# Performance work log

Measured on AMD Instinct MI355X. Metric: run time of the kernel, lower is better.

Reference implementation:

```python
import jax, jax.numpy as jnp
import numpy as np

B, S, D = 4, 2048, 2048


def setup_inputs() -> dict:
    key = jax.random.key(0)
    ks = jax.random.split(key, 9)
    scale = 1.0 / np.sqrt(D)
    x = jax.random.normal(ks[0], (B, S, D), dtype=jnp.float32)
    # causal mask, broadcast to [B, S, S]; 0 -> masked
    mask = jnp.broadcast_to(jnp.tril(jnp.ones((S, S), dtype=jnp.int32)), (B, S, S))
    Wq = jax.random.normal(ks[1], (D, D), dtype=jnp.float32) * scale
    Wk = jax.random.normal(ks[2], (D, D), dtype=jnp.float32) * scale
    Wv = jax.random.normal(ks[3], (D, D), dtype=jnp.float32) * scale
    Wp = jax.random.normal(ks[4], (D, D), dtype=jnp.float32) * scale
    bq = jnp.zeros((D,), jnp.float32)
    bk = jnp.zeros((D,), jnp.float32)
    bv = jnp.zeros((D,), jnp.float32)
    bp = jnp.zeros((D,), jnp.float32)
    return {"x": x, "mask": mask, "Wq": Wq, "bq": bq, "Wk": Wk, "bk": bk,
            "Wv": Wv, "bv": bv, "Wp": Wp, "bp": bp}


def reference(x, mask, Wq, bq, Wk, bk, Wv, bv, Wp, bp):
    # single-head scaled dot-product attention (cache=None path, eval mode)
    d_k = x.shape[-1]
    inv_std = 1.0 / jnp.sqrt(jnp.asarray(d_k, x.dtype))
    q = jnp.einsum('bsd,ed->bse', x, Wq) + bq  # nn.Linear: x @ W^T + b
    k = jnp.einsum('bsd,ed->bse', x, Wk) + bk
    v = jnp.einsum('bsd,ed->bse', x, Wv) + bv
    scores = jnp.einsum('bqd,bkd->bqk', q, k) * inv_std  # [B,S,S]
    scores = jnp.where(mask == 0, jnp.asarray(-jnp.inf, scores.dtype), scores)
    attn = jax.nn.softmax(scores, axis=-1)
    ctx = jnp.einsum('bqk,bkd->bqd', attn, v)
    out = jnp.einsum('bsd,ed->bse', ctx, Wp) + bp
    return out
```

## Files before the change

kernel.cpp:

```cpp
#include <hip/hip_runtime.h>
#include <hip/hip_bf16.h>
#include <type_traits>
#include <math.h>


typedef __bf16 bf16x8_t __attribute__((ext_vector_type(8)));
typedef float f32x4_t __attribute__((ext_vector_type(4)));
typedef unsigned short u16x8_t __attribute__((ext_vector_type(8)));

__device__ inline unsigned short f2bf(float f) {
  unsigned int u = __builtin_bit_cast(unsigned int, f);
  unsigned int r = u + 0x7fffu + ((u >> 16) & 1u);
  return (unsigned short)(r >> 16);
}

__device__ inline void gl2lds16(const unsigned short* g, unsigned short* l) {
  __builtin_amdgcn_global_load_lds(
      (const __attribute__((address_space(1))) unsigned int*)g,
      (__attribute__((address_space(3))) unsigned int*)l, 16, 0, 0);
}

__device__ __forceinline__ bf16x8_t ldf(const unsigned short* p) {
  return __builtin_bit_cast(bf16x8_t, *(const u16x8_t*)p);
}

#define MF(a_, b_, c_) \
  (c_) = __builtin_amdgcn_mfma_f32_16x16x32_bf16((a_), (b_), (c_), 0, 0, 0)
#define SB0() __builtin_amdgcn_sched_barrier(0)
#define BAR()                         \
  do {                                \
    SB0();                            \
    __builtin_amdgcn_s_barrier();     \
    SB0();                            \
  } while (0)
#define LGK0()                                  \
  do {                                          \
    asm volatile("s_waitcnt lgkmcnt(0)");       \
    SB0();                                      \
  } while (0)
#define VM4()                                   \
  do {                                          \
    asm volatile("s_waitcnt vmcnt(4)");         \
    SB0();                                      \
  } while (0)
#define VM6()                                   \
  do {                                          \
    asm volatile("s_waitcnt vmcnt(6)");         \
    SB0();                                      \
  } while (0)
#define PRIO(x) __builtin_amdgcn_s_setprio(x)

__global__ __launch_bounds__(256) void cast_f32_bf16(
    const float* __restrict__ in, unsigned short* __restrict__ out, long n4) {
  long i = blockIdx.x * 256L + threadIdx.x;
  if (i >= n4) return;
  float4 f = ((const float4*)in)[i];
  ushort4 u;
  u.x = f2bf(f.x); u.y = f2bf(f.y); u.z = f2bf(f.z); u.w = f2bf(f.w);
  ((ushort4*)out)[i] = u;
}

__global__ __launch_bounds__(256) void cast_w4(
    const float* __restrict__ w0, const float* __restrict__ w1,
    const float* __restrict__ w2, const float* __restrict__ w3,
    unsigned short* __restrict__ o0, unsigned short* __restrict__ o1,
    unsigned short* __restrict__ o2, unsigned short* __restrict__ o3,
    long n4) {
  long i = blockIdx.x * 256L + threadIdx.x;
  if (i >= n4) return;
  const float* in; unsigned short* out;
  switch (blockIdx.y) {
    case 0: in = w0; out = o0; break;
    case 1: in = w1; out = o1; break;
    case 2: in = w2; out = o2; break;
    default: in = w3; out = o3; break;
  }
  float4 f = ((const float4*)in)[i];
  ushort4 u;
  u.x = f2bf(f.x); u.y = f2bf(f.y); u.z = f2bf(f.z); u.w = f2bf(f.w);
  ((ushort4*)out)[i] = u;
}

__device__ __forceinline__ void g256_kloop(
    const unsigned short* __restrict__ A, const unsigned short* __restrict__ B,
    int K, int Keff, unsigned short* smem, f32x4_t (&acc)[8][4]) {
  const int tid = threadIdx.x;
  const int lane = tid & 63;
  const int wave = tid >> 6;
  const int wr = wave >> 2;
  const int wc = wave & 3;
  const int fr = lane & 15;
  const int q4 = lane >> 4;
  const int s0 = (q4 ^ (fr & 7)) * 8;
  const int s1 = ((q4 + 4) ^ (fr & 7)) * 8;
  const size_t rowK =
      (size_t)(wave * 8 + (lane >> 3)) * (size_t)K +
      (size_t)(((lane & 7) ^ ((lane >> 3) & 7)) * 8);
  const size_t K64 = (size_t)64 * K;
  const size_t K128 = (size_t)128 * K;
  const int wofs = wave * 512;
  const int NT = Keff >> 6;
  const int aoff = wr * 8192 + fr * 64;
  const int boff = 16384 + (wc >> 1) * 8192 + (wc & 1) * 4096 + fr * 64;

#define STG(gp_, lh_)                        \
  do {                                       \
    const unsigned short* g_ = (gp_) + rowK; \
    gl2lds16(g_, (lh_) + wofs);              \
    gl2lds16(g_ + K64, (lh_) + 4096 + wofs); \
  } while (0)

#define MFMA8(mb_, af_)                          \
  _Pragma("unroll")                              \
  for (int n = 0; n < 4; ++n) {                  \
    MF(af_[0][0], bfr[n][0], acc[(mb_)][n]);     \
    MF(af_[0][1], bfr[n][1], acc[(mb_)][n]);     \
    MF(af_[1][0], bfr[n][0], acc[(mb_) + 1][n]); \
    MF(af_[1][1], bfr[n][1], acc[(mb_) + 1][n]); \
  }

#define RDA(dst_, base_, mo_)                          \
  _Pragma("unroll")                                    \
  for (int m = 0; m < 2; ++m) {                        \
    dst_[m][0] = ldf((base_) + (m + (mo_)) * 1024 + s0); \
    dst_[m][1] = ldf((base_) + (m + (mo_)) * 1024 + s1); \
  }

  STG(A, smem);
  STG(A + K128, smem + 8192);
  STG(B, smem + 16384);
  STG(B + K128, smem + 24576);
  STG(B + 64, smem + 32768 + 16384);
  STG(B + K128 + 64, smem + 32768 + 24576);
  STG(A + 64, smem + 32768);
  VM6();
  BAR();

  bf16x8_t bfr[4][2], a01[2][2], a23[2][2], a45[2][2], a67[2][2];
  {
    const unsigned short* Bh = smem + boff;
    const unsigned short* Ah = smem + aoff;
#pragma unroll
    for (int n = 0; n < 4; ++n) {
      bfr[n][0] = ldf(Bh + n * 1024 + s0);
      bfr[n][1] = ldf(Bh + n * 1024 + s1);
    }
    RDA(a01, Ah, 0);
  }

  for (int kt = 0; kt < NT; ++kt) {
    unsigned short* bc = smem + ((kt & 1) << 15);
    unsigned short* nb = smem + (((kt + 1) & 1) << 15);
    const unsigned short* Ahc = bc + aoff;
    const unsigned short* Ahn = nb + aoff;
    const unsigned short* Bhn = nb + boff;
    int k1 = (kt + 1) << 6; if (k1 >= Keff) k1 -= Keff;
    int k2 = (kt + 2) << 6; if (k2 >= Keff) k2 -= Keff;

    RDA(a23, Ahc, 2);
    STG(A + K128 + k1, nb + 8192);
    BAR();
    PRIO(1);
    MFMA8(0, a01);
    PRIO(0);
    BAR();

    RDA(a45, Ahc, 4);
    STG(B + k2, bc + 16384);
    BAR();
    PRIO(1);
    MFMA8(2, a23);
    PRIO(0);
    BAR();

    RDA(a67, Ahc, 6);
    STG(B + K128 + k2, bc + 24576);
    BAR();
    PRIO(1);
    MFMA8(4, a45);
    PRIO(0);
    BAR();

    VM4();
    LGK0();
    BAR();
    STG(A + k2, bc);
    PRIO(1);
#pragma unroll
    for (int n = 0; n < 4; ++n) {
      MF(a67[0][0], bfr[n][0], acc[6][n]);
      MF(a67[0][1], bfr[n][1], acc[6][n]);
      MF(a67[1][0], bfr[n][0], acc[7][n]);
      MF(a67[1][1], bfr[n][1], acc[7][n]);
      bfr[n][0] = ldf(Bhn + n * 1024 + s0);
      bfr[n][1] = ldf(Bhn + n * 1024 + s1);
    }
    RDA(a01, Ahn, 0);
    PRIO(0);
    BAR();
  }
#undef STG
#undef MFMA8
#undef RDA
}

template <int MODE, typename OutT>
__global__ __launch_bounds__(512, 2) void gemm256_nt(
    const unsigned short* __restrict__ A, const unsigned short* __restrict__ B,
    OutT* __restrict__ C, const float* __restrict__ bias, float alpha,
    int N, int K, size_t sA, size_t sB, size_t sC) {
  int lin = blockIdx.y * gridDim.x + blockIdx.x;
  const int nwg = gridDim.x * gridDim.y;
  lin = (lin & 7) * (nwg >> 3) + (lin >> 3);
  const int bm = (lin / gridDim.x) * 256;
  const int bn = (lin % gridDim.x) * 256;
  if (MODE == 1 && bn >= bm + 256) return;
  int Keff = K;
  if (MODE == 2) { int kl = bm + 256; Keff = kl < K ? kl : K; }

  A += (size_t)blockIdx.z * sA + (size_t)bm * K;
  B += (size_t)blockIdx.z * sB + (size_t)bn * K;
  C += (size_t)blockIdx.z * sC;

  __shared__ unsigned short smem[65536];
  f32x4_t acc[8][4] = {};
  g256_kloop(A, B, K, Keff, smem, acc);

  const int tid = threadIdx.x;
  const int lane = tid & 63;
  const int wave = tid >> 6;
  const int wr = wave >> 2, wc = wave & 3;
  const int fr = lane & 15, q4 = lane >> 4;
  const int r0 = bm + wr * 128 + q4 * 4;
  const int c0 = bn + wc * 64 + fr;
#pragma unroll
  for (int n = 0; n < 4; ++n) {
    const int col = c0 + n * 16;
    const float bs = bias ? bias[col] : 0.f;
#pragma unroll
    for (int m = 0; m < 8; ++m) {
      const int row = r0 + m * 16;
#pragma unroll
      for (int r = 0; r < 4; ++r) {
        float v = acc[m][n][r] * alpha + bs;
        if constexpr (std::is_same_v<OutT, float>)
          C[(size_t)(row + r) * N + col] = v;
        else
          C[(size_t)(row + r) * N + col] = f2bf(v);
      }
    }
  }
}

__global__ __launch_bounds__(512, 2) void gemm256_qkv(
    const unsigned short* __restrict__ A, const unsigned short* __restrict__ Bw,
    unsigned short* __restrict__ Q, unsigned short* __restrict__ Kd,
    unsigned short* __restrict__ Vt,
    const float* __restrict__ bq, const float* __restrict__ bk,
    const float* __restrict__ bv, int K, int D, int S) {
  int lin = blockIdx.y * gridDim.x + blockIdx.x;
  const int nwg = gridDim.x * gridDim.y;
  lin = (lin & 7) * (nwg >> 3) + (lin >> 3);
  const int bm = (lin / gridDim.x) * 256;
  const int bn = (lin % gridDim.x) * 256;

  __shared__ unsigned short smem[65536];
  f32x4_t acc[8][4] = {};
  g256_kloop(A + (size_t)bm * K, Bw + (size_t)bn * K, K, K, smem, acc);

  const int tid = threadIdx.x;
  const int lane = tid & 63;
  const int wave = tid >> 6;
  const int wr = wave >> 2, wc = wave & 3;
  const int fr = lane & 15, q4 = lane >> 4;
  const int r0 = bm + wr * 128 + q4 * 4;
  const int c0 = bn + wc * 64 + fr;
#pragma unroll
  for (int n = 0; n < 4; ++n) {
    const int col = c0 + n * 16;
    const int sel = col >> 11;
    const int idx = col & (D - 1);
    const float bs = (sel == 0 ? bq : sel == 1 ? bk : bv)[idx];
#pragma unroll
    for (int m = 0; m < 8; ++m) {
      const int row = r0 + m * 16;
      if (sel < 2) {
        unsigned short* dst = sel == 0 ? Q : Kd;
#pragma unroll
        for (int r = 0; r < 4; ++r)
          dst[(size_t)(row + r) * D + idx] = f2bf(acc[m][n][r] + bs);
      } else {
        const int b = row >> 11;
        const int s = row & (S - 1);
        ushort4 pack;
        pack.x = f2bf(acc[m][n][0] + bs);
        pack.y = f2bf(acc[m][n][1] + bs);
        pack.z = f2bf(acc[m][n][2] + bs);
        pack.w = f2bf(acc[m][n][3] + bs);
        *(ushort4*)&Vt[(size_t)b * D * S + (size_t)idx * S + s] = pack;
      }
    }
  }
}

__global__ __launch_bounds__(256) void softmax_causal(
    const float* __restrict__ Sc, unsigned short* __restrict__ P, int n) {
  const int row = blockIdx.x;
  const int q = row & (n - 1);
  const float* srow = Sc + (size_t)row * n;
  unsigned short* prow = P + (size_t)row * n;
  const int tid = threadIdx.x, lane = tid & 63, wid = tid >> 6;
  __shared__ float red[4];

  float m = -3.0e38f;
  for (int j = tid; j <= q; j += 256) m = fmaxf(m, srow[j]);
#pragma unroll
  for (int o = 32; o; o >>= 1) m = fmaxf(m, __shfl_down(m, o, 64));
  if (lane == 0) red[wid] = m;
  __syncthreads();
  m = fmaxf(fmaxf(red[0], red[1]), fmaxf(red[2], red[3]));
  __syncthreads();

  float s = 0.f;
  for (int j = tid; j <= q; j += 256) s += __expf(srow[j] - m);
#pragma unroll
  for (int o = 32; o; o >>= 1) s += __shfl_down(s, o, 64);
  if (lane == 0) red[wid] = s;
  __syncthreads();
  s = red[0] + red[1] + red[2] + red[3];
  const float inv = 1.f / s;

  for (int j = tid; j < n; j += 256) {
    float v = (j <= q) ? __expf(srow[j] - m) * inv : 0.f;
    prow[j] = f2bf(v);
  }
}

extern "C" void kernel_launch(void* const* d_in, const int* in_sizes, int n_in,
                              void* d_out, int out_size, void* d_ws, size_t ws_size,
                              hipStream_t stream) {
  const int B = 4, S = 2048, D = 2048;
  const int M = B * S;

  const float* x  = (const float*)d_in[0];
  const float* Wq = (const float*)d_in[2];
  const float* bq = (const float*)d_in[3];
  const float* Wk = (const float*)d_in[4];
  const float* bk = (const float*)d_in[5];
  const float* Wv = (const float*)d_in[6];
  const float* bv = (const float*)d_in[7];
  const float* Wp = (const float*)d_in[8];
  const float* bp = (const float*)d_in[9];
  float* out = (float*)d_out;

  char* ws = (char*)d_ws;
  const size_t MB = 1ull << 20;
  unsigned short* xb   = (unsigned short*)(ws + 0);
  unsigned short* wqkv = (unsigned short*)(ws + 32 * MB);
  unsigned short* wpb  = (unsigned short*)(ws + 56 * MB);
  unsigned short* qb   = (unsigned short*)(ws + 64 * MB);
  unsigned short* kb   = (unsigned short*)(ws + 96 * MB);
  unsigned short* vtb  = (unsigned short*)(ws + 160 * MB);
  float*          sc   = (float*)(ws + 192 * MB);
  unsigned short* pb   = qb;
  unsigned short* cb   = kb;

  const long nx = (long)M * D;
  const long nw = (long)D * D;

  cast_f32_bf16<<<dim3((unsigned)((nx / 4 + 255) / 256)), 256, 0, stream>>>(x, xb, nx / 4);
  cast_w4<<<dim3((unsigned)((nw / 4 + 255) / 256), 4), 256, 0, stream>>>(
      Wq, Wk, Wv, Wp,
      wqkv, wqkv + (size_t)D * D, wqkv + 2 * (size_t)D * D, wpb, nw / 4);

  const dim3 blk(512);

  gemm256_qkv<<<dim3(3 * D / 256, M / 256), blk, 0, stream>>>(
      xb, wqkv, qb, kb, vtb, bq, bk, bv, D, D, S);

  const float inv_std = 1.f / sqrtf((float)D);
  gemm256_nt<1, float><<<dim3(S / 256, S / 256, B), blk, 0, stream>>>(
      qb, kb, sc, nullptr, inv_std, S, D, (size_t)S * D, (size_t)S * D, (size_t)S * S);

  softmax_causal<<<dim3(B * S), dim3(256), 0, stream>>>(sc, pb, S);

  gemm256_nt<2, unsigned short><<<dim3(D / 256, S / 256, B), blk, 0, stream>>>(
      pb, vtb, cb, nullptr, 1.f, D, S, (size_t)S * S, (size_t)D * S, (size_t)S * D);

  gemm256_nt<0, float><<<dim3(D / 256, M / 256), blk, 0, stream>>>(
      cb, wpb, out, bp, 1.f, D, D, 0, 0, 0);
}
```

Baseline: 617.7 us.

## Issue LDS fragment reads via inline ds_read_b128 with partial lgkmcnt waits

Replaces the compiler-generated LDS vector loads in the GEMM k-loop with inline-asm ds_read_b128 on byte-addressed LDS pointers. Explicit s_waitcnt lgkmcnt(4) waits before each MFMA block let the next fragment reads stay in flight while the current MFMAs run. The A-tile global-to-LDS stage is moved after the next-buffer fragment reads, and sched barriers pin the ordering. Because the compiler cannot see the asm loads' latency, correctness now depends entirely on the hand-placed waitcnts.

```diff
diff --git a/kernel.cpp b/kernel.cpp
--- a/kernel.cpp
+++ b/kernel.cpp
@@ -20,8 +20,15 @@
       (__attribute__((address_space(3))) unsigned int*)l, 16, 0, 0);
 }
 
-__device__ __forceinline__ bf16x8_t ldf(const unsigned short* p) {
-  return __builtin_bit_cast(bf16x8_t, *(const u16x8_t*)p);
+__device__ __forceinline__ unsigned as3base(const unsigned short* p) {
+  return (unsigned)(unsigned long long)
+      (const __attribute__((address_space(3))) unsigned short*)p;
+}
+
+__device__ __forceinline__ bf16x8_t ldsa(unsigned a) {
+  bf16x8_t r;
+  asm volatile("ds_read_b128 %0, %1" : "=v"(r) : "v"(a));
+  return r;
 }
 
 #define MF(a_, b_, c_) \
@@ -33,10 +40,10 @@
     __builtin_amdgcn_s_barrier();     \
     SB0();                            \
   } while (0)
-#define LGK0()                                  \
-  do {                                          \
-    asm volatile("s_waitcnt lgkmcnt(0)");       \
-    SB0();                                      \
+#define LGK(n_)                                          \
+  do {                                                   \
+    asm volatile("s_waitcnt lgkmcnt(" #n_ ")");          \
+    SB0();                                               \
   } while (0)
 #define VM4()                                   \
   do {                                          \
@@ -91,8 +98,8 @@
   const int wc = wave & 3;
   const int fr = lane & 15;
   const int q4 = lane >> 4;
-  const int s0 = (q4 ^ (fr & 7)) * 8;
-  const int s1 = ((q4 + 4) ^ (fr & 7)) * 8;
+  const unsigned s0b = (unsigned)((q4 ^ (fr & 7)) * 16);
+  const unsigned s1b = (unsigned)(((q4 + 4) ^ (fr & 7)) * 16);
   const size_t rowK =
       (size_t)(wave * 8 + (lane >> 3)) * (size_t)K +
       (size_t)(((lane & 7) ^ ((lane >> 3) & 7)) * 8);
@@ -100,8 +107,10 @@
   const size_t K128 = (size_t)128 * K;
   const int wofs = wave * 512;
   const int NT = Keff >> 6;
-  const int aoff = wr * 8192 + fr * 64;
-  const int boff = 16384 + (wc >> 1) * 8192 + (wc & 1) * 4096 + fr * 64;
+  const unsigned sb = as3base(smem);
+  const unsigned aoffB = (unsigned)(wr * 16384 + fr * 128);
+  const unsigned boffB =
+      (unsigned)(32768 + (wc >> 1) * 16384 + (wc & 1) * 8192 + fr * 128);
 
 #define STG(gp_, lh_)                        \
   do {                                       \
@@ -119,11 +128,11 @@
     MF(af_[1][1], bfr[n][1], acc[(mb_) + 1][n]); \
   }
 
-#define RDA(dst_, base_, mo_)                          \
-  _Pragma("unroll")                                    \
-  for (int m = 0; m < 2; ++m) {                        \
-    dst_[m][0] = ldf((base_) + (m + (mo_)) * 1024 + s0); \
-    dst_[m][1] = ldf((base_) + (m + (mo_)) * 1024 + s1); \
+#define RDA(dst_, baseB_, mo_)                                \
+  _Pragma("unroll")                                           \
+  for (int m = 0; m < 2; ++m) {                               \
+    dst_[m][0] = ldsa((baseB_) + (m + (mo_)) * 2048u + s0b);  \
+    dst_[m][1] = ldsa((baseB_) + (m + (mo_)) * 2048u + s1b);  \
   }
 
   STG(A, smem);
@@ -138,53 +147,58 @@
 
   bf16x8_t bfr[4][2], a01[2][2], a23[2][2], a45[2][2], a67[2][2];
   {
-    const unsigned short* Bh = smem + boff;
-    const unsigned short* Ah = smem + aoff;
+    const unsigned Bh = sb + boffB;
+    const unsigned Ah = sb + aoffB;
 #pragma unroll
     for (int n = 0; n < 4; ++n) {
-      bfr[n][0] = ldf(Bh + n * 1024 + s0);
-      bfr[n][1] = ldf(Bh + n * 1024 + s1);
+      bfr[n][0] = ldsa(Bh + n * 2048u + s0b);
+      bfr[n][1] = ldsa(Bh + n * 2048u + s1b);
     }
     RDA(a01, Ah, 0);
   }
 
   for (int kt = 0; kt < NT; ++kt) {
-    unsigned short* bc = smem + ((kt & 1) << 15);
-    unsigned short* nb = smem + (((kt + 1) & 1) << 15);
-    const unsigned short* Ahc = bc + aoff;
-    const unsigned short* Ahn = nb + aoff;
-    const unsigned short* Bhn = nb + boff;
+    unsigned short* bcp = smem + ((kt & 1) << 15);
+    unsigned short* nbp = smem + (((kt + 1) & 1) << 15);
+    const unsigned AhcB = sb + ((unsigned)(kt & 1) << 16) + aoffB;
+    const unsigned AhnB = sb + ((unsigned)((kt + 1) & 1) << 16) + aoffB;
+    const unsigned BhnB = sb + ((unsigned)((kt + 1) & 1) << 16) + boffB;
     int k1 = (kt + 1) << 6; if (k1 >= Keff) k1 -= Keff;
     int k2 = (kt + 2) << 6; if (k2 >= Keff) k2 -= Keff;
 
-    RDA(a23, Ahc, 2);
-    STG(A + K128 + k1, nb + 8192);
-    BAR();
+    RDA(a23, AhcB, 2);
+    SB0();
+    STG(A + K128 + k1, nbp + 8192);
+    BAR();
+    LGK(4);
     PRIO(1);
     MFMA8(0, a01);
     PRIO(0);
     BAR();
 
-    RDA(a45, Ahc, 4);
-    STG(B + k2, bc + 16384);
-    BAR();
+    RDA(a45, AhcB, 4);
+    SB0();
+    STG(B + k2, bcp + 16384);
+    BAR();
+    LGK(4);
     PRIO(1);
     MFMA8(2, a23);
     PRIO(0);
     BAR();
 
-    RDA(a67, Ahc, 6);
-    STG(B + K128 + k2, bc + 24576);
-    BAR();
+    RDA(a67, AhcB, 6);
+    SB0();
+    STG(B + K128 + k2, bcp + 24576);
+    BAR();
+    LGK(4);
     PRIO(1);
     MFMA8(4, a45);
     PRIO(0);
     BAR();
 
     VM4();
-    LGK0();
-    BAR();
-    STG(A + k2, bc);
+    LGK(0);
+    BAR();
     PRIO(1);
 #pragma unroll
     for (int n = 0; n < 4; ++n) {
@@ -192,11 +206,13 @@
       MF(a67[0][1], bfr[n][1], acc[6][n]);
       MF(a67[1][0], bfr[n][0], acc[7][n]);
       MF(a67[1][1], bfr[n][1], acc[7][n]);
-      bfr[n][0] = ldf(Bhn + n * 1024 + s0);
-      bfr[n][1] = ldf(Bhn + n * 1024 + s1);
+      bfr[n][0] = ldsa(BhnB + n * 2048u + s0b);
+      bfr[n][1] = ldsa(BhnB + n * 2048u + s1b);
     }
-    RDA(a01, Ahn, 0);
+    RDA(a01, AhnB, 0);
     PRIO(0);
+    SB0();
+    STG(A + k2, bcp);
     BAR();
   }
 #undef STG
```

Result: no change. 620.9 us (+0.5%).
